# Performance work log

Measured on AMD Instinct MI355X. Metric: run time of the kernel, lower is better.

Reference implementation:

```python
import jax, jax.numpy as jnp
import numpy as np

D = 1024
M = 16
H = D // M  # 64
EPS = 1e-05


def setup_inputs() -> dict:
    key = jax.random.key(0)
    ks = jax.random.split(key, 5)
    B, T = 4, 1024
    x = jax.random.normal(ks[0], (B, T, D), dtype=jnp.float32)
    norm_w = jnp.ones((D,), dtype=jnp.float32)
    s = 1.0 / np.sqrt(D)
    W_v = jax.random.uniform(ks[1], (D, D), dtype=jnp.float32, minval=-s, maxval=s)
    W_a = jax.random.uniform(ks[2], (H * M * (M + 1), D), dtype=jnp.float32, minval=-s, maxval=s)
    W_out = jax.random.uniform(ks[3], (D, D), dtype=jnp.float32, minval=-s, maxval=s)
    return {"x": x, "norm_w": norm_w, "W_v": W_v, "W_a": W_a, "W_out": W_out}


def _rmsnorm(x, w, eps=EPS):
    var = jnp.mean(jnp.square(x), axis=-1, keepdims=True)
    return x * jax.lax.rsqrt(var + eps) * w


def reference(x, norm_w, W_v, W_a, W_out):
    B, T, _ = x.shape
    h = _rmsnorm(x, norm_w)                              # [B,T,D]
    v = (h @ W_v.T).reshape(B, T, H, M)                  # [B,T,H,m]
    gate_logits = (h @ W_a.T).reshape(B, T, H, M, M + 1)
    gates = jax.nn.softmax(gate_logits, axis=-1)
    a0 = gates[..., 0]                                   # [B,T,H,m]
    A = gates[..., 1:]                                   # [B,T,H,m,m]

    # time-major for scan
    A_t = jnp.moveaxis(A, 1, 0)                          # [T,B,H,m,m]
    u_t = jnp.moveaxis(a0 * v, 1, 0)                     # [T,B,H,m]

    def step(state, inp):
        At, ut = inp
        new = jnp.einsum('bhij,bhj->bhi', At, state) + ut
        return new, new

    init = jnp.zeros((B, H, M), dtype=x.dtype)
    _, ys = jax.lax.scan(step, init, (A_t, u_t))         # ys: [T,B,H,m]
    h_out = jnp.moveaxis(ys, 0, 1).reshape(B, T, D)
    return x + h_out @ W_out.T
```

## Files before the change

kernel.cpp:

```cpp
#include <hip/hip_runtime.h>
#include <hip/hip_bf16.h>
#include <math.h>

#define B_DIM 4
#define T_DIM 1024
#define D_DIM 1024
#define M_DIM 16
#define H_DIM 64
#define NT    4096
#define NA    17408
#define NCAT  18432
#define EPSV  1e-5f
#define CL    16
#define NC    64

typedef __bf16 bf16_t;
typedef __bf16 bf16x4 __attribute__((ext_vector_type(4)));
typedef __bf16 bf16x8 __attribute__((ext_vector_type(8)));
typedef float  f32x4  __attribute__((ext_vector_type(4)));
typedef unsigned short u16;

#define PBAR() do { asm volatile("" ::: "memory"); __builtin_amdgcn_s_barrier(); asm volatile("" ::: "memory"); } while (0)
#define VM0()   do { asm volatile("s_waitcnt vmcnt(0)" ::: "memory"); __builtin_amdgcn_sched_barrier(0); } while (0)

__global__ __launch_bounds__(256) void prep_kernel(const float* __restrict__ x,
                                                   const float* __restrict__ nw,
                                                   const float* __restrict__ Wa,
                                                   const float* __restrict__ Wv,
                                                   const float* __restrict__ Wo,
                                                   bf16_t* __restrict__ h,
                                                   bf16_t* __restrict__ wcat,
                                                   bf16_t* __restrict__ wo) {
  int tid = threadIdx.x;
  if (blockIdx.x < NT) {
    int row = blockIdx.x;
    const float4* xr = reinterpret_cast<const float4*>(x + (size_t)row * D_DIM);
    float4 xv = xr[tid];
    float ss = xv.x * xv.x + xv.y * xv.y + xv.z * xv.z + xv.w * xv.w;
#pragma unroll
    for (int m = 1; m < 64; m <<= 1) ss += __shfl_xor(ss, m, 64);
    __shared__ float red[4];
    int lane = tid & 63, wid = tid >> 6;
    if (lane == 0) red[wid] = ss;
    __syncthreads();
    float tot = red[0] + red[1] + red[2] + red[3];
    float scale = rsqrtf(tot * (1.0f / D_DIM) + EPSV);
    float4 wv = reinterpret_cast<const float4*>(nw)[tid];
    bf16x4 o;
    o[0] = (bf16_t)(xv.x * scale * wv.x);
    o[1] = (bf16_t)(xv.y * scale * wv.y);
    o[2] = (bf16_t)(xv.z * scale * wv.z);
    o[3] = (bf16_t)(xv.w * scale * wv.w);
    reinterpret_cast<bf16x4*>(h)[(size_t)row * 256 + tid] = o;
  } else {
    constexpr int NA4 = NA * D_DIM / 4;
    constexpr int NV4 = D_DIM * D_DIM / 4;
    constexpr int total = NA4 + 2 * NV4;
    int nb = gridDim.x - NT;
    int idx = (blockIdx.x - NT) * 256 + tid;
    int stride = nb * 256;
    for (; idx < total; idx += stride) {
      const float* src; bf16_t* dst; int js, jd;
      if (idx < NA4) {
        src = Wa; dst = wcat; js = idx;
        int row = idx >> 8;
        int c4 = idx & 255;
        int hh = row / 272, r = row - hh * 272;
        int ii = r / 17, jj = r - ii * 17;
        int nrow = hh * 272 + jj * 16 + ii;
        jd = (nrow << 8) + c4;
      } else if (idx < NA4 + NV4) {
        src = Wv; dst = wcat + (size_t)NA * D_DIM; js = idx - NA4; jd = js;
      } else {
        src = Wo; dst = wo; js = idx - NA4 - NV4; jd = js;
      }
      float4 v = reinterpret_cast<const float4*>(src)[js];
      bf16x4 o;
      o[0] = (bf16_t)v.x; o[1] = (bf16_t)v.y; o[2] = (bf16_t)v.z; o[3] = (bf16_t)v.w;
      reinterpret_cast<bf16x4*>(dst)[jd] = o;
    }
  }
}

__global__ __launch_bounds__(256) void gemm_out_kernel(const bf16_t* __restrict__ A,
                                                       const bf16_t* __restrict__ Bw,
                                                       float* __restrict__ Cout,
                                                       const float* __restrict__ resid,
                                                       int Ndim, int K) {
  constexpr int BM = 128, BN = 128, BK = 32;
  __shared__ bf16_t As[BM * BK];
  __shared__ bf16_t Bs[BN * BK];

  int tid = threadIdx.x;
  int lane = tid & 63;
  int wid = tid >> 6;
  int wm = wid >> 1, wn = wid & 1;
  int bm = blockIdx.x * BM;
  int bn = blockIdx.y * BN;
  int l15 = lane & 15;
  int l4 = lane >> 4;

  f32x4 acc[4][4];
#pragma unroll
  for (int i = 0; i < 4; i++)
#pragma unroll
    for (int j = 0; j < 4; j++) acc[i][j] = (f32x4){0.f, 0.f, 0.f, 0.f};

  const bf16_t* Ag = A + (size_t)bm * K;
  const bf16_t* Bg = Bw + (size_t)bn * K;
  int srow_lane = lane >> 2;
  int scol = (lane & 3) * 8;

  for (int k0 = 0; k0 < K; k0 += BK) {
#pragma unroll
    for (int i = 0; i < 2; i++) {
      int rbase = wid * 32 + i * 16;
      int r = rbase + srow_lane;
      __builtin_amdgcn_global_load_lds(
          (const __attribute__((address_space(1))) void*)(Ag + (size_t)r * K + k0 + scol),
          (__attribute__((address_space(3))) void*)(As + rbase * BK), 16, 0, 0);
      __builtin_amdgcn_global_load_lds(
          (const __attribute__((address_space(1))) void*)(Bg + (size_t)r * K + k0 + scol),
          (__attribute__((address_space(3))) void*)(Bs + rbase * BK), 16, 0, 0);
    }
    __syncthreads();

    const bf16x8* Asv = reinterpret_cast<const bf16x8*>(As);
    const bf16x8* Bsv = reinterpret_cast<const bf16x8*>(Bs);
    bf16x8 af[4], bfr[4];
#pragma unroll
    for (int mf = 0; mf < 4; mf++)
      af[mf] = Asv[(wm * 64 + mf * 16 + l15) * 4 + l4];
#pragma unroll
    for (int nf = 0; nf < 4; nf++)
      bfr[nf] = Bsv[(wn * 64 + nf * 16 + l15) * 4 + l4];
#pragma unroll
    for (int mf = 0; mf < 4; mf++)
#pragma unroll
      for (int nf = 0; nf < 4; nf++)
        acc[mf][nf] = __builtin_amdgcn_mfma_f32_16x16x32_bf16(af[mf], bfr[nf], acc[mf][nf], 0, 0, 0);
    __syncthreads();
  }

#pragma unroll
  for (int mf = 0; mf < 4; mf++)
#pragma unroll
    for (int nf = 0; nf < 4; nf++)
#pragma unroll
      for (int i = 0; i < 4; i++) {
        int row = bm + wm * 64 + mf * 16 + l4 * 4 + i;
        int col = bn + wn * 64 + nf * 16 + l15;
        size_t idx = (size_t)row * Ndim + col;
        Cout[idx] = acc[mf][nf][i] + resid[idx];
      }
}

__global__ __launch_bounds__(512, 2) void gemm256_nt_kernel(const bf16_t* __restrict__ A,
                                                            const bf16_t* __restrict__ Bw,
                                                            bf16_t* __restrict__ Clg,
                                                            bf16_t* __restrict__ Cv) {
  constexpr int K = 1024;
  constexpr int G = K / 64;
  __shared__ bf16_t As[2 * 16384];
  __shared__ bf16_t Bs[2 * 16384];

  const int tid = threadIdx.x;
  const int lane = tid & 63;
  const int w = tid >> 6;
  const int wm = w >> 2;
  const int wn = w & 3;
  const int l15 = lane & 15;
  const int l4 = lane >> 4;

  const int bm = blockIdx.x * 256;
  const int bn = blockIdx.y * 256;

  const bf16_t* Ag = A + (size_t)bm * K;
  const bf16_t* Bg = Bw + (size_t)bn * K;

  int growi[2], gcoli[2];
#pragma unroll
  for (int j = 0; j < 2; ++j) {
    int E = j * 4096 + tid * 8;
    int sub = E >> 9, e = E & 511;
    int rin = e >> 5, cs = e & 31;
    int cin = cs ^ ((rin & 8) ? 16 : 0);
    growi[j] = (sub >> 1) * 16 + rin;
    gcoli[j] = (sub & 1) * 32 + cin;
  }

  const int fbase = l15 * 32 + ((l4 * 8) ^ ((l15 & 8) ? 16 : 0));

  f32x4 acc[8][4];
#pragma unroll
  for (int i = 0; i < 8; i++)
#pragma unroll
    for (int j = 0; j < 4; j++) acc[i][j] = (f32x4){0.f, 0.f, 0.f, 0.f};

  bf16x8 ALo[8], AHi[8], B0r[4], B1r[4];

  auto stageHalf = [&](const bf16_t* Gp, bf16_t* Lp, int bufp, int half, int t2) {
#pragma unroll
    for (int j = 0; j < 2; ++j) {
      const bf16_t* src = Gp + (size_t)(half * 128 + growi[j]) * K + t2 * 64 + gcoli[j];
      __builtin_amdgcn_global_load_lds(
          (const __attribute__((address_space(1))) void*)src,
          (__attribute__((address_space(3))) void*)(Lp + bufp * 16384 + half * 8192 + j * 4096 + w * 512),
          16, 0, 0);
    }
  };

  auto rdA4 = [&](bf16x8* dst, int bufp, int rgrpBase) {
    const bf16_t* base = As + bufp * 16384;
#pragma unroll
    for (int mf = 0; mf < 4; ++mf)
#pragma unroll
      for (int kk = 0; kk < 2; ++kk)
        dst[mf * 2 + kk] = *reinterpret_cast<const bf16x8*>(base + ((rgrpBase + mf) * 2 + kk) * 512 + fbase);
  };
  auto rdA2 = [&](bf16x8* dst, int bufp, int rgrpBase) {
    const bf16_t* base = As + bufp * 16384;
#pragma unroll
    for (int mf = 0; mf < 2; ++mf)
#pragma unroll
      for (int kk = 0; kk < 2; ++kk)
        dst[mf * 2 + kk] = *reinterpret_cast<const bf16x8*>(base + ((rgrpBase + mf) * 2 + kk) * 512 + fbase);
  };
  auto rdB = [&](bf16x8* dst, int bufp, int nfBase) {
    const bf16_t* base = Bs + bufp * 16384;
#pragma unroll
    for (int nf = 0; nf < 2; ++nf)
#pragma unroll
      for (int kk = 0; kk < 2; ++kk)
        dst[nf * 2 + kk] = *reinterpret_cast<const bf16x8*>(base + ((wn * 4 + nfBase + nf) * 2 + kk) * 512 + fbase);
  };
  auto MM = [&](const bf16x8* Af, const bf16x8* Bf, int mfB, int nfB) {
    __builtin_amdgcn_s_setprio(1);
#pragma unroll
    for (int mf = 0; mf < 4; ++mf)
#pragma unroll
      for (int nf = 0; nf < 2; ++nf)
#pragma unroll
        for (int kk = 0; kk < 2; ++kk)
          acc[mfB + mf][nfB + nf] = __builtin_amdgcn_mfma_f32_16x16x32_bf16(
              Af[mf * 2 + kk], Bf[nf * 2 + kk], acc[mfB + mf][nfB + nf], 0, 0, 0);
    __builtin_amdgcn_s_setprio(0);
  };

  stageHalf(Bg, Bs, 0, 0, 0);
  stageHalf(Bg, Bs, 0, 1, 0);
  stageHalf(Ag, As, 0, 0, 0);
  stageHalf(Ag, As, 0, 1, 0);
  stageHalf(Ag, As, 1, 0, 1);
  stageHalf(Ag, As, 1, 1, 1);
  asm volatile("s_waitcnt vmcnt(0)" ::: "memory");
  PBAR();
  rdA4(ALo, 0, wm * 8);

#pragma unroll 1
  for (int t = 0; t < G; ++t) {
    const int buf = t & 1;
    const int nbuf = buf ^ 1;

    rdB(B0r, buf, 0);
    rdA2(AHi, buf, wm * 8 + 4);
    if (t + 1 < G) stageHalf(Bg, Bs, nbuf, 0, t + 1);
    MM(ALo, B0r, 0, 0);
    PBAR();

    rdB(B1r, buf, 2);
    rdA2(AHi + 4, buf, wm * 8 + 6);
    if (t + 1 < G) stageHalf(Bg, Bs, nbuf, 1, t + 1);
    MM(ALo, B1r, 0, 2);
    if (t + 1 < G) asm volatile("s_waitcnt vmcnt(4)" ::: "memory");
    PBAR();

    if (t + 1 < G) rdA4(ALo, nbuf, wm * 8);
    if (t + 2 < G) stageHalf(Ag, As, buf, 0, t + 2);
    MM(AHi, B0r, 4, 0);
    PBAR();

    if (t + 2 < G) stageHalf(Ag, As, buf, 1, t + 2);
    MM(AHi, B1r, 4, 2);
    if (t + 2 < G)      asm volatile("s_waitcnt vmcnt(4)" ::: "memory");
    else if (t + 1 < G) asm volatile("s_waitcnt vmcnt(0)" ::: "memory");
    PBAR();
  }

  if (blockIdx.y < 68) {
#pragma unroll
    for (int mf = 0; mf < 8; ++mf)
#pragma unroll
      for (int nf = 0; nf < 4; ++nf)
#pragma unroll
        for (int i = 0; i < 4; ++i) {
          int row = bm + wm * 128 + mf * 16 + l4 * 4 + i;
          int col = bn + wn * 64 + nf * 16 + l15;
          Clg[(size_t)row * NA + col] = (bf16_t)acc[mf][nf][i];
        }
  } else {
    int cb = bn - NA;
#pragma unroll
    for (int mf = 0; mf < 8; ++mf)
#pragma unroll
      for (int nf = 0; nf < 4; ++nf)
#pragma unroll
        for (int i = 0; i < 4; ++i) {
          int row = bm + wm * 128 + mf * 16 + l4 * 4 + i;
          int col = cb + wn * 64 + nf * 16 + l15;
          Cv[(size_t)row * D_DIM + col] = (bf16_t)acc[mf][nf][i];
        }
  }
}

__device__ __forceinline__ void softmax17s(const bf16_t* __restrict__ bp, float vval,
                                           f32x4& a0, f32x4& a1, f32x4& a2, f32x4& a3,
                                           float& u) {
  const u16* lp = reinterpret_cast<const u16*>(bp);
  float e[17];
  float mx = -1e30f;
#pragma unroll
  for (int j = 0; j < 17; ++j) {
    e[j] = __uint_as_float(((unsigned)lp[j * 16]) << 16);
    mx = fmaxf(mx, e[j]);
  }
  float s = 0.f;
#pragma unroll
  for (int j = 0; j < 17; ++j) {
    e[j] = __expf(e[j] - mx);
    s += e[j];
  }
  float inv = 1.0f / s;
  a0 = (f32x4){e[1] * inv, e[2] * inv, e[3] * inv, e[4] * inv};
  a1 = (f32x4){e[5] * inv, e[6] * inv, e[7] * inv, e[8] * inv};
  a2 = (f32x4){e[9] * inv, e[10] * inv, e[11] * inv, e[12] * inv};
  a3 = (f32x4){e[13] * inv, e[14] * inv, e[15] * inv, e[16] * inv};
  u = e[0] * inv * vval;
}

__global__ __launch_bounds__(256) void scanA_kernel(const bf16_t* __restrict__ lg,
                                                    const bf16_t* __restrict__ v,
                                                    float* __restrict__ sum) {
  int bc = blockIdx.x;
  int b = bc >> 6;
  int c = bc & 63;
  int g = threadIdx.x >> 4;
  int i = threadIdx.x & 15;
  int h = blockIdx.y * 16 + g;
  int chain = b * 64 + h;
  int rbase = b * T_DIM + c * CL;

  __shared__ float Arows[16][16][16];
  __shared__ float Us[16][16];

  f32x4 R0 = (f32x4){i == 0 ? 1.f : 0.f, i == 1 ? 1.f : 0.f, i == 2 ? 1.f : 0.f, i == 3 ? 1.f : 0.f};
  f32x4 R1 = (f32x4){i == 4 ? 1.f : 0.f, i == 5 ? 1.f : 0.f, i == 6 ? 1.f : 0.f, i == 7 ? 1.f : 0.f};
  f32x4 R2 = (f32x4){i == 8 ? 1.f : 0.f, i == 9 ? 1.f : 0.f, i == 10 ? 1.f : 0.f, i == 11 ? 1.f : 0.f};
  f32x4 R3 = (f32x4){i == 12 ? 1.f : 0.f, i == 13 ? 1.f : 0.f, i == 14 ? 1.f : 0.f, i == 15 ? 1.f : 0.f};
  float q = 0.f;

#pragma unroll 1
  for (int tau = CL - 1; tau >= 0; --tau) {
    int r = rbase + tau;
    float vval = (float)v[(size_t)r * D_DIM + h * 16 + i];
    f32x4 a0, a1, a2, a3;
    float uu;
    softmax17s(lg + (size_t)r * NA + h * 272 + i, vval, a0, a1, a2, a3, uu);

    *reinterpret_cast<f32x4*>(&Arows[g][i][0]) = a0;
    *reinterpret_cast<f32x4*>(&Arows[g][i][4]) = a1;
    *reinterpret_cast<f32x4*>(&Arows[g][i][8]) = a2;
    *reinterpret_cast<f32x4*>(&Arows[g][i][12]) = a3;
    Us[g][i] = uu;
    asm volatile("s_waitcnt lgkmcnt(0)" ::: "memory");
    __builtin_amdgcn_sched_barrier(0);

    f32x4 u0 = *reinterpret_cast<const f32x4*>(&Us[g][0]);
    f32x4 u1 = *reinterpret_cast<const f32x4*>(&Us[g][4]);
    f32x4 u2 = *reinterpret_cast<const f32x4*>(&Us[g][8]);
    f32x4 u3 = *reinterpret_cast<const f32x4*>(&Us[g][12]);
    float qa = fmaf(R0[0], u0[0], fmaf(R0[1], u0[1], fmaf(R0[2], u0[2], R0[3] * u0[3])));
    float qb = fmaf(R1[0], u1[0], fmaf(R1[1], u1[1], fmaf(R1[2], u1[2], R1[3] * u1[3])));
    float qc = fmaf(R2[0], u2[0], fmaf(R2[1], u2[1], fmaf(R2[2], u2[2], R2[3] * u2[3])));
    float qd = fmaf(R3[0], u3[0], fmaf(R3[1], u3[1], fmaf(R3[2], u3[2], R3[3] * u3[3])));
    q += (qa + qb) + (qc + qd);

    f32x4 n0 = (f32x4){0.f, 0.f, 0.f, 0.f}, n1 = n0, n2 = n0, n3 = n0;
#pragma unroll
    for (int k = 0; k < 16; ++k) {
      float rk = (k < 4) ? R0[k & 3] : (k < 8) ? R1[k & 3] : (k < 12) ? R2[k & 3] : R3[k & 3];
      f32x4 b0 = *reinterpret_cast<const f32x4*>(&Arows[g][k][0]);
      f32x4 b1 = *reinterpret_cast<const f32x4*>(&Arows[g][k][4]);
      f32x4 b2 = *reinterpret_cast<const f32x4*>(&Arows[g][k][8]);
      f32x4 b3 = *reinterpret_cast<const f32x4*>(&Arows[g][k][12]);
#pragma unroll
      for (int e2 = 0; e2 < 4; ++e2) {
        n0[e2] = fmaf(rk, b0[e2], n0[e2]);
        n1[e2] = fmaf(rk, b1[e2], n1[e2]);
        n2[e2] = fmaf(rk, b2[e2], n2[e2]);
        n3[e2] = fmaf(rk, b3[e2], n3[e2]);
      }
    }
    R0 = n0; R1 = n1; R2 = n2; R3 = n3;
  }

  float* sp = sum + (size_t)(chain * NC + c) * 272;
  *reinterpret_cast<f32x4*>(&sp[i * 16 + 0]) = R0;
  *reinterpret_cast<f32x4*>(&sp[i * 16 + 4]) = R1;
  *reinterpret_cast<f32x4*>(&sp[i * 16 + 8]) = R2;
  *reinterpret_cast<f32x4*>(&sp[i * 16 + 12]) = R3;
  sp[256 + i] = q;
}

__global__ __launch_bounds__(64) void scanB_kernel(const float* __restrict__ sum,
                                                   float* __restrict__ sinit) {
  int chain = blockIdx.x;
  int lane = threadIdx.x;
  int i = lane & 15;

  __shared__ float seg[2][2176];

  const float* gbase = sum + (size_t)chain * NC * 272;

  auto load_seg = [&](int s, int buf) {
#pragma unroll
    for (int r = 0; r < 9; ++r) {
      int idx = r * 256 + lane * 4;
      if (idx < 2176) {
        __builtin_amdgcn_global_load_lds(
            (const __attribute__((address_space(1))) void*)(gbase + (size_t)s * 2176 + idx),
            (__attribute__((address_space(3))) void*)(&seg[buf][r * 256]), 16, 0, 0);
      }
    }
  };

  load_seg(0, 0);
  VM0();

  f32x4 S0 = (f32x4){0.f, 0.f, 0.f, 0.f}, S1 = S0, S2 = S0, S3 = S0;
  float own = 0.f;

  for (int sg = 0; sg < 8; ++sg) {
    int buf = sg & 1;
    if (sg + 1 < 8) load_seg(sg + 1, buf ^ 1);
#pragma unroll 1
    for (int cc = 0; cc < 8; ++cc) {
      int c = sg * 8 + cc;
      const float* Pb = &seg[buf][cc * 272];
      if (lane < 16) sinit[(size_t)(chain * NC + c) * 16 + i] = own;

      f32x4 p0 = *reinterpret_cast<const f32x4*>(&Pb[i * 16 + 0]);
      f32x4 p1 = *reinterpret_cast<const f32x4*>(&Pb[i * 16 + 4]);
      f32x4 p2 = *reinterpret_cast<const f32x4*>(&Pb[i * 16 + 8]);
      f32x4 p3 = *reinterpret_cast<const f32x4*>(&Pb[i * 16 + 12]);
      float qq = Pb[256 + i];

      float pa = fmaf(p0[0], S0[0], fmaf(p0[1], S0[1], fmaf(p0[2], S0[2], p0[3] * S0[3])));
      float pb = fmaf(p1[0], S1[0], fmaf(p1[1], S1[1], fmaf(p1[2], S1[2], p1[3] * S1[3])));
      float pc = fmaf(p2[0], S2[0], fmaf(p2[1], S2[1], fmaf(p2[2], S2[2], p2[3] * S2[3])));
      float pd = fmaf(p3[0], S3[0], fmaf(p3[1], S3[1], fmaf(p3[2], S3[2], p3[3] * S3[3])));
      float p = (pa + pb) + (pc + pd) + qq;
      own = p;

#pragma unroll
      for (int j = 0; j < 4; ++j) {
        S0[j] = __shfl(p, j, 64);
        S1[j] = __shfl(p, 4 + j, 64);
        S2[j] = __shfl(p, 8 + j, 64);
        S3[j] = __shfl(p, 12 + j, 64);
      }
    }
    if (sg + 1 < 8) VM0();
  }
}

__global__ __launch_bounds__(256) void scanC_kernel(const bf16_t* __restrict__ lg,
                                                    const bf16_t* __restrict__ v,
                                                    const float* __restrict__ sinit,
                                                    bf16_t* __restrict__ y) {
  int bc = blockIdx.x;
  int b = bc >> 6;
  int c = bc & 63;
  int g = threadIdx.x >> 4;
  int i = threadIdx.x & 15;
  int h = blockIdx.y * 16 + g;
  int chain = b * 64 + h;
  int rbase = b * T_DIM + c * CL;

  __shared__ float Sb[16][16];

  const float* ip = sinit + (size_t)(chain * NC + c) * 16;
  f32x4 S0 = *reinterpret_cast<const f32x4*>(&ip[0]);
  f32x4 S1 = *reinterpret_cast<const f32x4*>(&ip[4]);
  f32x4 S2 = *reinterpret_cast<const f32x4*>(&ip[8]);
  f32x4 S3 = *reinterpret_cast<const f32x4*>(&ip[12]);

#pragma unroll 1
  for (int t = 0; t < CL; ++t) {
    int r = rbase + t;
    float vval = (float)v[(size_t)r * D_DIM + h * 16 + i];
    f32x4 a0, a1, a2, a3;
    float uu;
    softmax17s(lg + (size_t)r * NA + h * 272 + i, vval, a0, a1, a2, a3, uu);

    float pa = fmaf(a0[0], S0[0], fmaf(a0[1], S0[1], fmaf(a0[2], S0[2], a0[3] * S0[3])));
    float pb = fmaf(a1[0], S1[0], fmaf(a1[1], S1[1], fmaf(a1[2], S1[2], a1[3] * S1[3])));
    float pc = fmaf(a2[0], S2[0], fmaf(a2[1], S2[1], fmaf(a2[2], S2[2], a2[3] * S2[3])));
    float pd = fmaf(a3[0], S3[0], fmaf(a3[1], S3[1], fmaf(a3[2], S3[2], a3[3] * S3[3])));
    float p = (pa + pb) + (pc + pd) + uu;

    y[(size_t)r * D_DIM + h * 16 + i] = (bf16_t)p;

    Sb[g][i] = p;
    asm volatile("s_waitcnt lgkmcnt(0)" ::: "memory");
    __builtin_amdgcn_sched_barrier(0);
    S0 = *reinterpret_cast<const f32x4*>(&Sb[g][0]);
    S1 = *reinterpret_cast<const f32x4*>(&Sb[g][4]);
    S2 = *reinterpret_cast<const f32x4*>(&Sb[g][8]);
    S3 = *reinterpret_cast<const f32x4*>(&Sb[g][12]);
  }
}

extern "C" void kernel_launch(void* const* d_in, const int* in_sizes, int n_in,
                              void* d_out, int out_size, void* d_ws, size_t ws_size,
                              hipStream_t stream) {
  const float* x      = (const float*)d_in[0];
  const float* norm_w = (const float*)d_in[1];
  const float* W_v    = (const float*)d_in[2];
  const float* W_a    = (const float*)d_in[3];
  const float* W_out  = (const float*)d_in[4];

  char* ws = (char*)d_ws;
  size_t off = 0;
  auto alloc = [&](size_t bytes) {
    void* p = ws + off;
    off += (bytes + 255) & ~(size_t)255;
    return p;
  };
  bf16_t* wcat = (bf16_t*)alloc((size_t)NCAT * D_DIM * 2);
  bf16_t* wo_b = (bf16_t*)alloc((size_t)D_DIM * D_DIM * 2);
  bf16_t* h_b  = (bf16_t*)alloc((size_t)NT * D_DIM * 2);
  bf16_t* v_b  = (bf16_t*)alloc((size_t)NT * D_DIM * 2);
  bf16_t* lg_b = (bf16_t*)alloc((size_t)NT * NA * 2);
  bf16_t* y_b  = (bf16_t*)alloc((size_t)NT * D_DIM * 2);
  float*  sum_f   = (float*)alloc((size_t)256 * NC * 272 * 4);
  float*  sinit_f = (float*)alloc((size_t)256 * NC * 16 * 4);

  prep_kernel<<<NT + 2048, 256, 0, stream>>>(x, norm_w, W_a, W_v, W_out,
                                             h_b, wcat, wo_b);

  gemm256_nt_kernel<<<dim3(NT / 256, NCAT / 256), 512, 0, stream>>>(h_b, wcat, lg_b, v_b);

  scanA_kernel<<<dim3(256, 4), 256, 0, stream>>>(lg_b, v_b, sum_f);
  scanB_kernel<<<256, 64, 0, stream>>>(sum_f, sinit_f);
  scanC_kernel<<<dim3(256, 4), 256, 0, stream>>>(lg_b, v_b, sinit_f, y_b);

  gemm_out_kernel<<<dim3(NT / 128, D_DIM / 128), 256, 0, stream>>>(
      y_b, wo_b, (float*)d_out, x, D_DIM, D_DIM);
}
```

Baseline: 327.1 us.

## Drop redundant GEMM barriers, pad scan LDS arrays, remove explicit LDS waits

Removes two of the four workgroup barriers per iteration in the double-buffered GEMM main loop. It also pads the per-group LDS regions in the scan kernels (264-float and 20-float strides) to reduce bank conflicts. The explicit lgkmcnt waits and sched barriers between the LDS writes and reads are dropped, leaving ordering to the compiler. Fewer barriers risks read/write races on shared buffers in the GEMM. Dropping the waits relies on intra-wavefront LDS ordering for correctness.

```diff
diff --git a/kernel.cpp b/kernel.cpp
--- a/kernel.cpp
+++ b/kernel.cpp
@@ -266,7 +266,6 @@
     rdA2(AHi, buf, wm * 8 + 4);
     if (t + 1 < G) stageHalf(Bg, Bs, nbuf, 0, t + 1);
     MM(ALo, B0r, 0, 0);
-    PBAR();
 
     rdB(B1r, buf, 2);
     rdA2(AHi + 4, buf, wm * 8 + 6);
@@ -278,7 +277,6 @@
     if (t + 1 < G) rdA4(ALo, nbuf, wm * 8);
     if (t + 2 < G) stageHalf(Ag, As, buf, 0, t + 2);
     MM(AHi, B0r, 4, 0);
-    PBAR();
 
     if (t + 2 < G) stageHalf(Ag, As, buf, 1, t + 2);
     MM(AHi, B1r, 4, 2);
@@ -337,6 +335,8 @@
   a3 = (f32x4){e[13] * inv, e[14] * inv, e[15] * inv, e[16] * inv};
   u = e[0] * inv * vval;
 }
+
+#define AGS 264
 
 __global__ __launch_bounds__(256) void scanA_kernel(const bf16_t* __restrict__ lg,
                                                     const bf16_t* __restrict__ v,
@@ -350,8 +350,11 @@
   int chain = b * 64 + h;
   int rbase = b * T_DIM + c * CL;
 
-  __shared__ float Arows[16][16][16];
-  __shared__ float Us[16][16];
+  __shared__ float Arows[16 * AGS];
+  __shared__ float Us[16 * 20];
+
+  float* Ag_ = Arows + g * AGS;
+  float* Ug_ = Us + g * 20;
 
   f32x4 R0 = (f32x4){i == 0 ? 1.f : 0.f, i == 1 ? 1.f : 0.f, i == 2 ? 1.f : 0.f, i == 3 ? 1.f : 0.f};
   f32x4 R1 = (f32x4){i == 4 ? 1.f : 0.f, i == 5 ? 1.f : 0.f, i == 6 ? 1.f : 0.f, i == 7 ? 1.f : 0.f};
@@ -367,18 +370,16 @@
     float uu;
     softmax17s(lg + (size_t)r * NA + h * 272 + i, vval, a0, a1, a2, a3, uu);
 
-    *reinterpret_cast<f32x4*>(&Arows[g][i][0]) = a0;
-    *reinterpret_cast<f32x4*>(&Arows[g][i][4]) = a1;
-    *reinterpret_cast<f32x4*>(&Arows[g][i][8]) = a2;
-    *reinterpret_cast<f32x4*>(&Arows[g][i][12]) = a3;
-    Us[g][i] = uu;
-    asm volatile("s_waitcnt lgkmcnt(0)" ::: "memory");
-    __builtin_amdgcn_sched_barrier(0);
-
-    f32x4 u0 = *reinterpret_cast<const f32x4*>(&Us[g][0]);
-    f32x4 u1 = *reinterpret_cast<const f32x4*>(&Us[g][4]);
-    f32x4 u2 = *reinterpret_cast<const f32x4*>(&Us[g][8]);
-    f32x4 u3 = *reinterpret_cast<const f32x4*>(&Us[g][12]);
+    *reinterpret_cast<f32x4*>(&Ag_[i * 16 + 0]) = a0;
+    *reinterpret_cast<f32x4*>(&Ag_[i * 16 + 4]) = a1;
+    *reinterpret_cast<f32x4*>(&Ag_[i * 16 + 8]) = a2;
+    *reinterpret_cast<f32x4*>(&Ag_[i * 16 + 12]) = a3;
+    Ug_[i] = uu;
+
+    f32x4 u0 = *reinterpret_cast<const f32x4*>(&Ug_[0]);
+    f32x4 u1 = *reinterpret_cast<const f32x4*>(&Ug_[4]);
+    f32x4 u2 = *reinterpret_cast<const f32x4*>(&Ug_[8]);
+    f32x4 u3 = *reinterpret_cast<const f32x4*>(&Ug_[12]);
     float qa = fmaf(R0[0], u0[0], fmaf(R0[1], u0[1], fmaf(R0[2], u0[2], R0[3] * u0[3])));
     float qb = fmaf(R1[0], u1[0], fmaf(R1[1], u1[1], fmaf(R1[2], u1[2], R1[3] * u1[3])));
     float qc = fmaf(R2[0], u2[0], fmaf(R2[1], u2[1], fmaf(R2[2], u2[2], R2[3] * u2[3])));
@@ -389,10 +390,10 @@
 #pragma unroll
     for (int k = 0; k < 16; ++k) {
       float rk = (k < 4) ? R0[k & 3] : (k < 8) ? R1[k & 3] : (k < 12) ? R2[k & 3] : R3[k & 3];
-      f32x4 b0 = *reinterpret_cast<const f32x4*>(&Arows[g][k][0]);
-      f32x4 b1 = *reinterpret_cast<const f32x4*>(&Arows[g][k][4]);
-      f32x4 b2 = *reinterpret_cast<const f32x4*>(&Arows[g][k][8]);
-      f32x4 b3 = *reinterpret_cast<const f32x4*>(&Arows[g][k][12]);
+      f32x4 b0 = *reinterpret_cast<const f32x4*>(&Ag_[k * 16 + 0]);
+      f32x4 b1 = *reinterpret_cast<const f32x4*>(&Ag_[k * 16 + 4]);
+      f32x4 b2 = *reinterpret_cast<const f32x4*>(&Ag_[k * 16 + 8]);
+      f32x4 b3 = *reinterpret_cast<const f32x4*>(&Ag_[k * 16 + 12]);
 #pragma unroll
       for (int e2 = 0; e2 < 4; ++e2) {
         n0[e2] = fmaf(rk, b0[e2], n0[e2]);
@@ -487,7 +488,7 @@
   int chain = b * 64 + h;
   int rbase = b * T_DIM + c * CL;
 
-  __shared__ float Sb[16][16];
+  __shared__ float Sb[16][20];
 
   const float* ip = sinit + (size_t)(chain * NC + c) * 16;
   f32x4 S0 = *reinterpret_cast<const f32x4*>(&ip[0]);
@@ -512,8 +513,6 @@
     y[(size_t)r * D_DIM + h * 16 + i] = (bf16_t)p;
 
     Sb[g][i] = p;
-    asm volatile("s_waitcnt lgkmcnt(0)" ::: "memory");
-    __builtin_amdgcn_sched_barrier(0);
     S0 = *reinterpret_cast<const f32x4*>(&Sb[g][0]);
     S1 = *reinterpret_cast<const f32x4*>(&Sb[g][4]);
     S2 = *reinterpret_cast<const f32x4*>(&Sb[g][8]);
```

Measured after the change: 311.6 us. 4.7% less time.
